# Kernel optimization log

Measured on AMD Instinct MI355X. Metric: run time of the kernel, lower is better.

## Reference

```python
import jax, jax.numpy as jnp
import numpy as np

COMMITMENT_COST = 0.25
EMBEDDING_COST = 1.0


def setup_inputs() -> dict:
    key = jax.random.key(0)
    k1, k2 = jax.random.split(key)
    x = jax.random.normal(k1, (64, 1024, 64), dtype=jnp.float32)
    embeddings = jax.random.normal(k2, (1024, 64), dtype=jnp.float32)
    return {"x": x, "embeddings": embeddings}


def reference(x, embeddings):
    D = embeddings.shape[1]
    flat_x = x.reshape(-1, D)  # [N, D]
    distances = (
        jnp.sum(flat_x ** 2, axis=1, keepdims=True)
        + jnp.sum(embeddings ** 2, axis=1)
        - 2.0 * flat_x @ embeddings.T
    )
    encoding_indices = jnp.argmin(distances, axis=1)  # [N]
    quantized = embeddings[encoding_indices].reshape(x.shape)
    q_latent_loss = jnp.mean((quantized - jax.lax.stop_gradient(x)) ** 2) * EMBEDDING_COST
    e_latent_loss = jnp.mean((x - jax.lax.stop_gradient(quantized)) ** 2) * COMMITMENT_COST
    loss = q_latent_loss + e_latent_loss
    # Straight-through estimator
    quantized_st = x + jax.lax.stop_gradient(quantized - x)
    return (quantized_st, loss)
```

## Files before the change

### kernel.cpp

```cpp
#include <hip/hip_runtime.h>
#include <math.h>

#define NROWS 65536
#define D 64
#define K 1024
#define Q 4
#define CPB 256
#define RPB 256
#define T1 512
#define TAU_S 0.005f
#define LOSS_SCALE (1.25f / (65536.0f * 64.0f))

typedef short bf16x8 __attribute__((ext_vector_type(8)));
typedef float f32x4 __attribute__((ext_vector_type(4)));
typedef __attribute__((address_space(1))) const unsigned int glb_u32;
typedef __attribute__((address_space(3))) unsigned int lds_u32;

__device__ inline unsigned short f2bf(float f) {
    unsigned int u = __float_as_uint(f);
    unsigned int r = u + 0x7fffu + ((u >> 16) & 1u);
    return (unsigned short)(r >> 16);
}
__device__ inline float bf2f(unsigned short h) {
    return __uint_as_float(((unsigned int)h) << 16);
}
__device__ inline void cvt8(const float4& a, const float4& b, bf16x8& h, bf16x8& l) {
    float f[8] = {a.x, a.y, a.z, a.w, b.x, b.y, b.z, b.w};
#pragma unroll
    for (int j = 0; j < 8; ++j) {
        unsigned short hb = f2bf(f[j]);
        h[j] = (short)hb;
        l[j] = (short)f2bf(f[j] - bf2f(hb));
    }
}

#define MFMA __builtin_amdgcn_mfma_f32_16x16x32_bf16

__global__ void vq_prep(const float* __restrict__ E, float* __restrict__ Ch,
                        bf16x8* __restrict__ Eswz, float* __restrict__ lossp) {
    int k = blockIdx.x * blockDim.x + threadIdx.x;
    if (k == 0) *lossp = 0.f;
    if (k >= K) return;
    const float4* ev = (const float4*)(E + (size_t)k * D);
    float4 v4[16];
    float s = 0.f;
#pragma unroll
    for (int p = 0; p < 16; ++p) {
        float4 v = ev[p];
        v4[p] = v;
        s = fmaf(v.x, v.x, s); s = fmaf(v.y, v.y, s);
        s = fmaf(v.z, v.z, s); s = fmaf(v.w, v.w, s);
    }
    Ch[k] = 0.5f * s;
    int ct = k >> 4, li = k & 15;
#pragma unroll
    for (int kt = 0; kt < 2; ++kt)
#pragma unroll
        for (int o = 0; o < 4; ++o) {
            int lane = li + 16 * o;
            bf16x8 h, l;
            cvt8(v4[kt * 8 + o * 2], v4[kt * 8 + o * 2 + 1], h, l);
            Eswz[(size_t)(ct * 4 + kt * 2 + 0) * 64 + lane] = h;
            Eswz[(size_t)(ct * 4 + kt * 2 + 1) * 64 + lane] = l;
        }
}

__global__ __launch_bounds__(T1, 4) void vq_part(
    const float* __restrict__ X, const float* __restrict__ Chg,
    const bf16x8* __restrict__ Eswz,
    float* __restrict__ pm, float* __restrict__ pm2, int* __restrict__ pk)
{
    __shared__ bf16x8 sBuf[4096];
    __shared__ float  sCh[CPB];

    const int t    = threadIdx.x;
    const int w    = t >> 6;
    const int lane = t & 63;
    const int l15  = lane & 15;
    const int l4   = lane >> 4;
    const int q    = blockIdx.x & 3;
    const int rg   = blockIdx.x >> 2;

#pragma unroll
    for (int i = 0; i < 8; ++i) {
        int s = w * 8 + i;
        const bf16x8* gs = Eswz + ((size_t)q * 4096 + s * 64 + lane);
        __builtin_amdgcn_global_load_lds((glb_u32*)gs, (lds_u32*)(sBuf + s * 64), 16, 0, 0);
    }
    if (t < CPB) sCh[t] = Chg[q * CPB + t];

    const float4* Xg4 = (const float4*)X;
    bf16x8 ah[2][2], al[2][2];
#pragma unroll
    for (int rt = 0; rt < 2; ++rt) {
        size_t ab = ((size_t)rg * RPB + w * 32 + rt * 16 + l15) * 16;
#pragma unroll
        for (int kt = 0; kt < 2; ++kt) {
            float4 fa = Xg4[ab + kt * 8 + l4 * 2];
            float4 fb = Xg4[ab + kt * 8 + l4 * 2 + 1];
            cvt8(fa, fb, ah[rt][kt], al[rt][kt]);
        }
    }

    float m[2][4], m2[2][4]; int bk[2][4];
#pragma unroll
    for (int rt = 0; rt < 2; ++rt)
#pragma unroll
        for (int r = 0; r < 4; ++r) { m[rt][r] = -INFINITY; m2[rt][r] = -INFINITY; bk[rt][r] = 0; }

    __syncthreads();

#pragma unroll 2
    for (int ct = 0; ct < 16; ++ct) {
        bf16x8 bh0 = sBuf[ct * 256 +   0 + lane];
        bf16x8 bl0 = sBuf[ct * 256 +  64 + lane];
        bf16x8 bh1 = sBuf[ct * 256 + 128 + lane];
        bf16x8 bl1 = sBuf[ct * 256 + 192 + lane];
        float ce = sCh[ct * 16 + l15];

        f32x4 a0 = {-ce, -ce, -ce, -ce};
        f32x4 a1 = {-ce, -ce, -ce, -ce};
        __builtin_amdgcn_s_setprio(1);
        a0 = MFMA(ah[0][0], bh0, a0, 0, 0, 0); a1 = MFMA(ah[1][0], bh0, a1, 0, 0, 0);
        a0 = MFMA(ah[0][1], bh1, a0, 0, 0, 0); a1 = MFMA(ah[1][1], bh1, a1, 0, 0, 0);
        a0 = MFMA(al[0][0], bh0, a0, 0, 0, 0); a1 = MFMA(al[1][0], bh0, a1, 0, 0, 0);
        a0 = MFMA(al[0][1], bh1, a0, 0, 0, 0); a1 = MFMA(al[1][1], bh1, a1, 0, 0, 0);
        a0 = MFMA(ah[0][0], bl0, a0, 0, 0, 0); a1 = MFMA(ah[1][0], bl0, a1, 0, 0, 0);
        a0 = MFMA(ah[0][1], bl1, a0, 0, 0, 0); a1 = MFMA(ah[1][1], bl1, a1, 0, 0, 0);
        __builtin_amdgcn_s_setprio(0);

        const int kk = q * CPB + ct * 16 + l15;
#pragma unroll
        for (int r = 0; r < 4; ++r) {
            float v;
            v = a0[r];
            m2[0][r] = __builtin_amdgcn_fmed3f(m2[0][r], m[0][r], v);
            bk[0][r] = (v > m[0][r]) ? kk : bk[0][r];
            m[0][r]  = fmaxf(m[0][r], v);
            v = a1[r];
            m2[1][r] = __builtin_amdgcn_fmed3f(m2[1][r], m[1][r], v);
            bk[1][r] = (v > m[1][r]) ? kk : bk[1][r];
            m[1][r]  = fmaxf(m[1][r], v);
        }
    }

#pragma unroll
    for (int rt = 0; rt < 2; ++rt)
#pragma unroll
        for (int r = 0; r < 4; ++r) {
            float mm = m[rt][r], mm2 = m2[rt][r]; int kk = bk[rt][r];
#pragma unroll
            for (int off = 1; off < 16; off <<= 1) {
                float om  = __shfl_xor(mm,  off, 64);
                float om2 = __shfl_xor(mm2, off, 64);
                int   ok  = __shfl_xor(kk,  off, 64);
                mm2 = fmaxf(fmaxf(mm2, om2), fminf(mm, om));
                if (om > mm || (om == mm && ok < kk)) { mm = om; kk = ok; }
            }
            if (l15 == 0) {
                int grow = rg * RPB + w * 32 + rt * 16 + l4 * 4 + r;
                pm [q * NROWS + grow] = mm;
                pm2[q * NROWS + grow] = mm2;
                pk [q * NROWS + grow] = kk;
            }
        }
}

__global__ __launch_bounds__(256) void vq_comb(
    const float* __restrict__ X, const float* __restrict__ E,
    const float* __restrict__ Chg,
    const float* __restrict__ pm, const float* __restrict__ pm2,
    const int* __restrict__ pk,
    float* __restrict__ out, float* __restrict__ lossp)
{
    __shared__ int   sIdx[64], sFlag[64];
    __shared__ int   sNf;
    __shared__ float sLoss[4];
    const int t = threadIdx.x, w = t >> 6, lane = t & 63;
    if (t == 0) sNf = 0;
    __syncthreads();

    const float4* Xg4 = (const float4*)X;
    const float4* Eg4 = (const float4*)E;

    if (t < 64) {
        int row = blockIdx.x * 64 + t;
        float top = -INFINITY, sec = -INFINITY, m2w = -INFINITY; int kw = 0;
#pragma unroll
        for (int q = 0; q < 4; ++q) {
            float mq  = pm [q * NROWS + row];
            float m2q = pm2[q * NROWS + row];
            int   kq  = pk [q * NROWS + row];
            if (mq > top) { sec = top; top = mq; kw = kq; m2w = m2q; }
            else sec = fmaxf(sec, mq);
        }
        sec = fmaxf(sec, m2w);
        sIdx[t] = kw;
        if (top - sec < TAU_S) {
            int pos = atomicAdd(&sNf, 1);
            sFlag[pos] = t;
        }
    }
    __syncthreads();

    {
        int nf = sNf;
        for (int i = w; i < nf; i += 4) {
            int lr = sFlag[i];
            size_t grow = (size_t)blockIdx.x * 64 + lr;
            const float4* xr = Xg4 + grow * 16;
            float bs = -INFINITY; int bki = 0;
#pragma unroll 1
            for (int jj = 0; jj < 16; ++jj) {
                int kq = jj * 64 + lane;
                const float4* er = Eg4 + (size_t)kq * 16;
                float a0 = 0.f, a1 = 0.f, a2 = 0.f, a3 = 0.f;
#pragma unroll
                for (int p = 0; p < 16; p += 4) {
                    float4 xv0 = xr[p],     e0 = er[p];
                    float4 xv1 = xr[p + 1], e1 = er[p + 1];
                    float4 xv2 = xr[p + 2], e2 = er[p + 2];
                    float4 xv3 = xr[p + 3], e3 = er[p + 3];
                    a0 = fmaf(xv0.x, e0.x, a0); a0 = fmaf(xv0.y, e0.y, a0);
                    a0 = fmaf(xv0.z, e0.z, a0); a0 = fmaf(xv0.w, e0.w, a0);
                    a1 = fmaf(xv1.x, e1.x, a1); a1 = fmaf(xv1.y, e1.y, a1);
                    a1 = fmaf(xv1.z, e1.z, a1); a1 = fmaf(xv1.w, e1.w, a1);
                    a2 = fmaf(xv2.x, e2.x, a2); a2 = fmaf(xv2.y, e2.y, a2);
                    a2 = fmaf(xv2.z, e2.z, a2); a2 = fmaf(xv2.w, e2.w, a2);
                    a3 = fmaf(xv3.x, e3.x, a3); a3 = fmaf(xv3.y, e3.y, a3);
                    a3 = fmaf(xv3.z, e3.z, a3); a3 = fmaf(xv3.w, e3.w, a3);
                }
                float sv = ((a0 + a1) + (a2 + a3)) - Chg[kq];
                if (sv > bs) { bs = sv; bki = kq; }
            }
#pragma unroll
            for (int off = 1; off < 64; off <<= 1) {
                float ob = __shfl_xor(bs, off, 64);
                int  okk = __shfl_xor(bki, off, 64);
                if (ob > bs || (ob == bs && okk < bki)) { bs = ob; bki = okk; }
            }
            if (lane == 0) sIdx[lr] = bki;
        }
    }
    __syncthreads();

    {
        int row = t >> 2, q4 = t & 3;
        int kb = sIdx[row];
        size_t grow = (size_t)blockIdx.x * 64 + row;
        const float4* eq   = Eg4 + (size_t)kb * 16;
        const float4* xrow = Xg4 + grow * 16;
        float4* orow = (float4*)out + grow * 16;
        float ls = 0.f;
#pragma unroll
        for (int j = 0; j < 4; ++j) {
            int u = q4 * 4 + j;
            float4 qv = eq[u];
            float4 xv = xrow[u];
            orow[u] = qv;
            float dx = qv.x - xv.x; ls = fmaf(dx, dx, ls);
            float dy = qv.y - xv.y; ls = fmaf(dy, dy, ls);
            float dz = qv.z - xv.z; ls = fmaf(dz, dz, ls);
            float dw = qv.w - xv.w; ls = fmaf(dw, dw, ls);
        }
#pragma unroll
        for (int off = 32; off > 0; off >>= 1) ls += __shfl_down(ls, off, 64);
        if (lane == 0) sLoss[w] = ls;
        __syncthreads();
        if (t == 0)
            atomicAdd(lossp, (sLoss[0] + sLoss[1] + sLoss[2] + sLoss[3]) * LOSS_SCALE);
    }
}

extern "C" void kernel_launch(void* const* d_in, const int* in_sizes, int n_in,
                              void* d_out, int out_size, void* d_ws, size_t ws_size,
                              hipStream_t stream) {
    const float* X = (const float*)d_in[0];
    const float* E = (const float*)d_in[1];
    float* out   = (float*)d_out;
    float* lossp = out + (size_t)NROWS * D;

    float*  Ch   = (float*)d_ws;
    bf16x8* Eswz = (bf16x8*)((char*)d_ws + 4096);
    float*  pm   = (float*)((char*)d_ws + 4096 + 262144);
    float*  pm2  = pm + (size_t)Q * NROWS;
    int*    pk   = (int*)(pm2 + (size_t)Q * NROWS);

    vq_prep<<<(K + 255) / 256, 256, 0, stream>>>(E, Ch, Eswz, lossp);

    vq_part<<<(NROWS / RPB) * Q, T1, 0, stream>>>(X, Ch, Eswz, pm, pm2, pk);

    vq_comb<<<NROWS / 64, 256, 0, stream>>>(X, E, Ch, pm, pm2, pk, out, lossp);
}
```

Baseline: 87.85 us.

## Halve codebook LDS staging for occupancy and derive loss from precomputed distances

```diff
diff --git a/kernel.cpp b/kernel.cpp
--- a/kernel.cpp
+++ b/kernel.cpp
@@ -65,12 +65,12 @@
         }
 }
 
-__global__ __launch_bounds__(T1, 4) void vq_part(
+__global__ __launch_bounds__(T1, 8) void vq_part(
     const float* __restrict__ X, const float* __restrict__ Chg,
-    const bf16x8* __restrict__ Eswz,
+    const bf16x8* __restrict__ Eswz, float* __restrict__ rx,
     float* __restrict__ pm, float* __restrict__ pm2, int* __restrict__ pk)
 {
-    __shared__ bf16x8 sBuf[4096];
+    __shared__ bf16x8 sBuf[2048];
     __shared__ float  sCh[CPB];
 
     const int t    = threadIdx.x;
@@ -81,12 +81,19 @@
     const int q    = blockIdx.x & 3;
     const int rg   = blockIdx.x >> 2;
 
-#pragma unroll
-    for (int i = 0; i < 8; ++i) {
-        int s = w * 8 + i;
-        const bf16x8* gs = Eswz + ((size_t)q * 4096 + s * 64 + lane);
-        __builtin_amdgcn_global_load_lds((glb_u32*)gs, (lds_u32*)(sBuf + s * 64), 16, 0, 0);
-    }
+#define STAGE(c)                                                                     \
+    {                                                                                \
+        _Pragma("unroll")                                                            \
+        for (int i = 0; i < 4; ++i) {                                                \
+            int s = w * 4 + i;                                                       \
+            const bf16x8* gs = Eswz + ((size_t)q * 4096 + (size_t)(c) * 2048 +       \
+                                       s * 64 + lane);                               \
+            __builtin_amdgcn_global_load_lds((glb_u32*)gs,                           \
+                                             (lds_u32*)(sBuf + s * 64), 16, 0, 0);   \
+        }                                                                            \
+    }
+
+    STAGE(0);
     if (t < CPB) sCh[t] = Chg[q * CPB + t];
 
     const float4* Xg4 = (const float4*)X;
@@ -94,12 +101,21 @@
 #pragma unroll
     for (int rt = 0; rt < 2; ++rt) {
         size_t ab = ((size_t)rg * RPB + w * 32 + rt * 16 + l15) * 16;
+        float nrm = 0.f;
 #pragma unroll
         for (int kt = 0; kt < 2; ++kt) {
             float4 fa = Xg4[ab + kt * 8 + l4 * 2];
             float4 fb = Xg4[ab + kt * 8 + l4 * 2 + 1];
+            nrm = fmaf(fa.x, fa.x, nrm); nrm = fmaf(fa.y, fa.y, nrm);
+            nrm = fmaf(fa.z, fa.z, nrm); nrm = fmaf(fa.w, fa.w, nrm);
+            nrm = fmaf(fb.x, fb.x, nrm); nrm = fmaf(fb.y, fb.y, nrm);
+            nrm = fmaf(fb.z, fb.z, nrm); nrm = fmaf(fb.w, fb.w, nrm);
             cvt8(fa, fb, ah[rt][kt], al[rt][kt]);
         }
+        nrm += __shfl_xor(nrm, 16, 64);
+        nrm += __shfl_xor(nrm, 32, 64);
+        if (q == 0 && l4 == 0)
+            rx[rg * RPB + w * 32 + rt * 16 + l15] = nrm;
     }
 
     float m[2][4], m2[2][4]; int bk[2][4];
@@ -110,37 +126,44 @@
 
     __syncthreads();
 
+    for (int c = 0; c < 2; ++c) {
 #pragma unroll 2
-    for (int ct = 0; ct < 16; ++ct) {
-        bf16x8 bh0 = sBuf[ct * 256 +   0 + lane];
-        bf16x8 bl0 = sBuf[ct * 256 +  64 + lane];
-        bf16x8 bh1 = sBuf[ct * 256 + 128 + lane];
-        bf16x8 bl1 = sBuf[ct * 256 + 192 + lane];
-        float ce = sCh[ct * 16 + l15];
-
-        f32x4 a0 = {-ce, -ce, -ce, -ce};
-        f32x4 a1 = {-ce, -ce, -ce, -ce};
-        __builtin_amdgcn_s_setprio(1);
-        a0 = MFMA(ah[0][0], bh0, a0, 0, 0, 0); a1 = MFMA(ah[1][0], bh0, a1, 0, 0, 0);
-        a0 = MFMA(ah[0][1], bh1, a0, 0, 0, 0); a1 = MFMA(ah[1][1], bh1, a1, 0, 0, 0);
-        a0 = MFMA(al[0][0], bh0, a0, 0, 0, 0); a1 = MFMA(al[1][0], bh0, a1, 0, 0, 0);
-        a0 = MFMA(al[0][1], bh1, a0, 0, 0, 0); a1 = MFMA(al[1][1], bh1, a1, 0, 0, 0);
-        a0 = MFMA(ah[0][0], bl0, a0, 0, 0, 0); a1 = MFMA(ah[1][0], bl0, a1, 0, 0, 0);
-        a0 = MFMA(ah[0][1], bl1, a0, 0, 0, 0); a1 = MFMA(ah[1][1], bl1, a1, 0, 0, 0);
-        __builtin_amdgcn_s_setprio(0);
-
-        const int kk = q * CPB + ct * 16 + l15;
-#pragma unroll
-        for (int r = 0; r < 4; ++r) {
-            float v;
-            v = a0[r];
-            m2[0][r] = __builtin_amdgcn_fmed3f(m2[0][r], m[0][r], v);
-            bk[0][r] = (v > m[0][r]) ? kk : bk[0][r];
-            m[0][r]  = fmaxf(m[0][r], v);
-            v = a1[r];
-            m2[1][r] = __builtin_amdgcn_fmed3f(m2[1][r], m[1][r], v);
-            bk[1][r] = (v > m[1][r]) ? kk : bk[1][r];
-            m[1][r]  = fmaxf(m[1][r], v);
+        for (int ct = 0; ct < 8; ++ct) {
+            bf16x8 bh0 = sBuf[ct * 256 +   0 + lane];
+            bf16x8 bl0 = sBuf[ct * 256 +  64 + lane];
+            bf16x8 bh1 = sBuf[ct * 256 + 128 + lane];
+            bf16x8 bl1 = sBuf[ct * 256 + 192 + lane];
+            float ce = sCh[c * 128 + ct * 16 + l15];
+
+            f32x4 a0 = {-ce, -ce, -ce, -ce};
+            f32x4 a1 = {-ce, -ce, -ce, -ce};
+            __builtin_amdgcn_s_setprio(1);
+            a0 = MFMA(ah[0][0], bh0, a0, 0, 0, 0); a1 = MFMA(ah[1][0], bh0, a1, 0, 0, 0);
+            a0 = MFMA(ah[0][1], bh1, a0, 0, 0, 0); a1 = MFMA(ah[1][1], bh1, a1, 0, 0, 0);
+            a0 = MFMA(al[0][0], bh0, a0, 0, 0, 0); a1 = MFMA(al[1][0], bh0, a1, 0, 0, 0);
+            a0 = MFMA(al[0][1], bh1, a0, 0, 0, 0); a1 = MFMA(al[1][1], bh1, a1, 0, 0, 0);
+            a0 = MFMA(ah[0][0], bl0, a0, 0, 0, 0); a1 = MFMA(ah[1][0], bl0, a1, 0, 0, 0);
+            a0 = MFMA(ah[0][1], bl1, a0, 0, 0, 0); a1 = MFMA(ah[1][1], bl1, a1, 0, 0, 0);
+            __builtin_amdgcn_s_setprio(0);
+
+            const int kk = q * CPB + c * 128 + ct * 16 + l15;
+#pragma unroll
+            for (int r = 0; r < 4; ++r) {
+                float v;
+                v = a0[r];
+                m2[0][r] = __builtin_amdgcn_fmed3f(m2[0][r], m[0][r], v);
+                bk[0][r] = (v > m[0][r]) ? kk : bk[0][r];
+                m[0][r]  = fmaxf(m[0][r], v);
+                v = a1[r];
+                m2[1][r] = __builtin_amdgcn_fmed3f(m2[1][r], m[1][r], v);
+                bk[1][r] = (v > m[1][r]) ? kk : bk[1][r];
+                m[1][r]  = fmaxf(m[1][r], v);
+            }
+        }
+        if (c == 0) {
+            __syncthreads();
+            STAGE(1);
+            __syncthreads();
         }
     }
 
@@ -168,14 +191,13 @@
 
 __global__ __launch_bounds__(256) void vq_comb(
     const float* __restrict__ X, const float* __restrict__ E,
-    const float* __restrict__ Chg,
+    const float* __restrict__ Chg, const float* __restrict__ rx,
     const float* __restrict__ pm, const float* __restrict__ pm2,
     const int* __restrict__ pk,
     float* __restrict__ out, float* __restrict__ lossp)
 {
-    __shared__ int   sIdx[64], sFlag[64];
-    __shared__ int   sNf;
-    __shared__ float sLoss[4];
+    __shared__ int sIdx[64], sFlag[64];
+    __shared__ int sNf;
     const int t = threadIdx.x, w = t >> 6, lane = t & 63;
     if (t == 0) sNf = 0;
     __syncthreads();
@@ -183,6 +205,7 @@
     const float4* Xg4 = (const float4*)X;
     const float4* Eg4 = (const float4*)E;
 
+    float ls = 0.f;
     if (t < 64) {
         int row = blockIdx.x * 64 + t;
         float top = -INFINITY, sec = -INFINITY, m2w = -INFINITY; int kw = 0;
@@ -199,7 +222,14 @@
         if (top - sec < TAU_S) {
             int pos = atomicAdd(&sNf, 1);
             sFlag[pos] = t;
-        }
+        } else {
+            ls = fmaf(-2.f, top, rx[row]);
+        }
+    }
+    if (w == 0) {
+#pragma unroll
+        for (int off = 32; off > 0; off >>= 1) ls += __shfl_down(ls, off, 64);
+        if (lane == 0) atomicAdd(lossp, ls * LOSS_SCALE);
     }
     __syncthreads();
 
@@ -239,7 +269,10 @@
                 int  okk = __shfl_xor(bki, off, 64);
                 if (ob > bs || (ob == bs && okk < bki)) { bs = ob; bki = okk; }
             }
-            if (lane == 0) sIdx[lr] = bki;
+            if (lane == 0) {
+                sIdx[lr] = bki;
+                atomicAdd(lossp, fmaf(-2.f, bs, rx[grow]) * LOSS_SCALE);
+            }
         }
     }
     __syncthreads();
@@ -248,27 +281,13 @@
         int row = t >> 2, q4 = t & 3;
         int kb = sIdx[row];
         size_t grow = (size_t)blockIdx.x * 64 + row;
-        const float4* eq   = Eg4 + (size_t)kb * 16;
-        const float4* xrow = Xg4 + grow * 16;
+        const float4* eq = Eg4 + (size_t)kb * 16;
         float4* orow = (float4*)out + grow * 16;
-        float ls = 0.f;
 #pragma unroll
         for (int j = 0; j < 4; ++j) {
             int u = q4 * 4 + j;
-            float4 qv = eq[u];
-            float4 xv = xrow[u];
-            orow[u] = qv;
-            float dx = qv.x - xv.x; ls = fmaf(dx, dx, ls);
-            float dy = qv.y - xv.y; ls = fmaf(dy, dy, ls);
-            float dz = qv.z - xv.z; ls = fmaf(dz, dz, ls);
-            float dw = qv.w - xv.w; ls = fmaf(dw, dw, ls);
-        }
-#pragma unroll
-        for (int off = 32; off > 0; off >>= 1) ls += __shfl_down(ls, off, 64);
-        if (lane == 0) sLoss[w] = ls;
-        __syncthreads();
-        if (t == 0)
-            atomicAdd(lossp, (sLoss[0] + sLoss[1] + sLoss[2] + sLoss[3]) * LOSS_SCALE);
+            orow[u] = eq[u];
+        }
     }
 }
 
@@ -285,10 +304,11 @@
     float*  pm   = (float*)((char*)d_ws + 4096 + 262144);
     float*  pm2  = pm + (size_t)Q * NROWS;
     int*    pk   = (int*)(pm2 + (size_t)Q * NROWS);
+    float*  rx   = (float*)(pk + (size_t)Q * NROWS);
 
     vq_prep<<<(K + 255) / 256, 256, 0, stream>>>(E, Ch, Eswz, lossp);
 
-    vq_part<<<(NROWS / RPB) * Q, T1, 0, stream>>>(X, Ch, Eswz, pm, pm2, pk);
-
-    vq_comb<<<NROWS / 64, 256, 0, stream>>>(X, E, Ch, pm, pm2, pk, out, lossp);
-}
+    vq_part<<<(NROWS / RPB) * Q, T1, 0, stream>>>(X, Ch, Eswz, rx, pm, pm2, pk);
+
+    vq_comb<<<NROWS / 64, 256, 0, stream>>>(X, E, Ch, rx, pm, pm2, pk, out, lossp);
+}
```

Result: slower. 270.8 us (+208.2%).
